# Kernel optimization log

Hardware: AMD Instinct MI355X
Metric: run time of the kernel (lower is better)

The kernel has to match this reference:

```python
import jax, jax.numpy as jnp
import numpy as np


def setup_inputs() -> dict:
    key = jax.random.key(0)
    k1, = jax.random.split(key, 1)
    x = jax.random.normal(k1, (16, 512, 64, 64), dtype=jnp.float32)
    gamma = jnp.zeros((1,), dtype=jnp.float32)
    return {"x": x, "gamma": gamma}


def reference(x, gamma):
    B, C, H, W = x.shape
    q = x.reshape(B, C, H * W)              # B x C x N
    # energy: B x C x C  (channel-channel gram matrix)
    energy = jnp.einsum('bcn,bdn->bcd', q, q)
    # max-subtract transform: max over last dim minus energy
    energy_new = jnp.max(energy, axis=-1, keepdims=True) - energy
    attention = jax.nn.softmax(energy_new, axis=-1)  # B x C x C
    out = jnp.einsum('bcd,bdn->bcn', attention, q).reshape(B, C, H, W)
    return gamma * out + x
```

## Files before the change

### kernel.cpp

```cpp
#include <hip/hip_runtime.h>
#include <stdint.h>

#define B_ 16
#define C_ 512
#define N_ 4096

typedef float f32x4 __attribute__((ext_vector_type(4)));
typedef __bf16 bf16x8 __attribute__((ext_vector_type(8)));

static __device__ __forceinline__ unsigned short f2bf(float f) {
    unsigned int u = __float_as_uint(f);
    u += 0x7fffu + ((u >> 16) & 1u);
    return (unsigned short)(u >> 16);
}

static __device__ __forceinline__ void gload_lds16(const void* g, void* l) {
    __builtin_amdgcn_global_load_lds(
        (__attribute__((address_space(1))) unsigned int*)(g),
        (__attribute__((address_space(3))) unsigned int*)(l),
        16, 0, 0);
}

static __device__ __forceinline__ void stage_pair(const char* Ab, const char* Bb,
                                                  char* as, char* bs, int tid,
                                                  int rowBytes, int m0, int n0, int kByte) {
#pragma unroll
    for (int i = 0; i < 2; ++i) {
        int o = (i * 256 + tid) * 16;
        int mrow = o >> 6, inrow = o & 63;
        gload_lds16(Ab + (size_t)(m0 + mrow) * rowBytes + kByte + inrow, as + o);
        gload_lds16(Bb + (size_t)(n0 + mrow) * rowBytes + kByte + inrow, bs + o);
    }
}

__global__ __launch_bounds__(256)
void convert_transpose(const float* __restrict__ x,
                       unsigned short* __restrict__ q16,
                       unsigned short* __restrict__ qt16) {
    int b = blockIdx.z;
    int t = threadIdx.x;
    int c0 = blockIdx.y * 64 + (t >> 4) * 4;
    int n0 = blockIdx.x * 64 + (t & 15) * 4;

    const float* xb = x + ((size_t)b * C_ + c0) * N_ + n0;
    unsigned short h[4][4];
#pragma unroll
    for (int i = 0; i < 4; ++i) {
        float4 v = *(const float4*)(xb + (size_t)i * N_);
        h[i][0] = f2bf(v.x); h[i][1] = f2bf(v.y);
        h[i][2] = f2bf(v.z); h[i][3] = f2bf(v.w);
    }
    unsigned short* qb = q16 + ((size_t)b * C_ + c0) * N_ + n0;
#pragma unroll
    for (int i = 0; i < 4; ++i) {
        ushort4 p; p.x = h[i][0]; p.y = h[i][1]; p.z = h[i][2]; p.w = h[i][3];
        *(ushort4*)(qb + (size_t)i * N_) = p;
    }
    unsigned short* qtb = qt16 + ((size_t)b * N_ + n0) * C_ + c0;
#pragma unroll
    for (int j = 0; j < 4; ++j) {
        ushort4 p; p.x = h[0][j]; p.y = h[1][j]; p.z = h[2][j]; p.w = h[3][j];
        *(ushort4*)(qtb + (size_t)j * C_) = p;
    }
}

template<int KROW, int NT>
__global__ __launch_bounds__(256)
void gemm_bt_energy(const unsigned short* __restrict__ q16,
                    float* __restrict__ e0, float* __restrict__ e1) {
    int zb = blockIdx.z;
    int b = zb >> 1, ks = zb & 1;
    int kbeg = ks * (NT * 32);
    const char* Ab = (const char*)(q16 + (size_t)b * C_ * KROW);
    int m0 = blockIdx.y * 128, n0 = blockIdx.x * 128;

    __shared__ unsigned short As[3][128 * 32];
    __shared__ unsigned short Bs[3][128 * 32];

    int t = threadIdx.x;
    int lane = t & 63, wave = t >> 6;
    int wm = (wave >> 1) * 64, wn = (wave & 1) * 64;
    int qd = lane >> 4, r = lane & 15;

    f32x4 acc[4][4] = {};

    const int rowB = KROW * 2;
    stage_pair(Ab, Ab, (char*)As[0], (char*)Bs[0], t, rowB, m0, n0, kbeg * 2);
    stage_pair(Ab, Ab, (char*)As[1], (char*)Bs[1], t, rowB, m0, n0, (kbeg + 32) * 2);

    int bufi = 0;
    for (int tt = 0; tt < NT; ++tt) {
        if (tt < NT - 1) asm volatile("s_waitcnt vmcnt(4) lgkmcnt(0)" ::: "memory");
        else             asm volatile("s_waitcnt vmcnt(0) lgkmcnt(0)" ::: "memory");
        __builtin_amdgcn_s_barrier();

        if (tt + 2 < NT) {
            int nb = bufi + 2; if (nb >= 3) nb -= 3;
            stage_pair(Ab, Ab, (char*)As[nb], (char*)Bs[nb], t, rowB,
                       m0, n0, (kbeg + (tt + 2) * 32) * 2);
        }

        const unsigned short* as = As[bufi];
        const unsigned short* bs = Bs[bufi];
        bf16x8 af[4], bfr[4];
#pragma unroll
        for (int i = 0; i < 4; ++i)
            af[i] = *(const bf16x8*)&as[(wm + i * 16 + r) * 32 + qd * 8];
#pragma unroll
        for (int j = 0; j < 4; ++j)
            bfr[j] = *(const bf16x8*)&bs[(wn + j * 16 + r) * 32 + qd * 8];

        __builtin_amdgcn_s_setprio(1);
#pragma unroll
        for (int i = 0; i < 4; ++i)
#pragma unroll
            for (int j = 0; j < 4; ++j)
                acc[i][j] = __builtin_amdgcn_mfma_f32_16x16x32_bf16(af[i], bfr[j], acc[i][j], 0, 0, 0);
        __builtin_amdgcn_s_setprio(0);

        if (++bufi == 3) bufi = 0;
    }

    float* Db = (ks ? e1 : e0) + (size_t)b * C_ * C_;
#pragma unroll
    for (int i = 0; i < 4; ++i)
#pragma unroll
        for (int j = 0; j < 4; ++j) {
            int row = m0 + wm + i * 16 + qd * 4;
            int col = n0 + wn + j * 16 + r;
#pragma unroll
            for (int rr = 0; rr < 4; ++rr)
                Db[(size_t)(row + rr) * C_ + col] = acc[i][j][rr];
        }
}

__global__ __launch_bounds__(256)
void softmax_neg(const float* __restrict__ e0, const float* __restrict__ e1,
                 unsigned short* __restrict__ att) {
    size_t row = blockIdx.x;
    const float* a = e0 + row * C_;
    const float* c = e1 + row * C_;
    int t = threadIdx.x;

    float x0 = a[t] + c[t], x1 = a[t + 256] + c[t + 256];
    float m = fminf(x0, x1);
#pragma unroll
    for (int off = 32; off > 0; off >>= 1) m = fminf(m, __shfl_down(m, off, 64));
    __shared__ float red[8];
    if ((t & 63) == 0) red[t >> 6] = m;
    __syncthreads();
    m = fminf(fminf(red[0], red[1]), fminf(red[2], red[3]));

    float p0 = __expf(m - x0), p1 = __expf(m - x1);
    float s = p0 + p1;
#pragma unroll
    for (int off = 32; off > 0; off >>= 1) s += __shfl_down(s, off, 64);
    if ((t & 63) == 0) red[4 + (t >> 6)] = s;
    __syncthreads();
    s = red[4] + red[5] + red[6] + red[7];
    float inv = 1.0f / s;

    att[row * C_ + t]       = f2bf(p0 * inv);
    att[row * C_ + t + 256] = f2bf(p1 * inv);
}

__global__ __launch_bounds__(256)
void gemm_bt_out(const unsigned short* __restrict__ att,
                 const unsigned short* __restrict__ qt16,
                 const float* __restrict__ x,
                 const float* __restrict__ gamma,
                 float* __restrict__ y) {
    const int K = 512;
    const int NT = K / 32;
    int b = blockIdx.z;
    const char* Ab = (const char*)(att  + (size_t)b * C_ * K);
    const char* Bb = (const char*)(qt16 + (size_t)b * N_ * K);
    int m0 = blockIdx.y * 128;
    int n0 = blockIdx.x * 128;

    __shared__ unsigned short As[3][128 * 32];
    __shared__ unsigned short Bs[3][128 * 32];

    int t = threadIdx.x;
    int lane = t & 63, wave = t >> 6;
    int wm = (wave >> 1) * 64, wn = (wave & 1) * 64;
    int qd = lane >> 4, r = lane & 15;

    f32x4 acc[4][4] = {};

    const int rowB = K * 2;
    stage_pair(Ab, Bb, (char*)As[0], (char*)Bs[0], t, rowB, m0, n0, 0);
    stage_pair(Ab, Bb, (char*)As[1], (char*)Bs[1], t, rowB, m0, n0, 64);

    int bufi = 0;
    for (int tt = 0; tt < NT; ++tt) {
        if (tt < NT - 1) asm volatile("s_waitcnt vmcnt(4) lgkmcnt(0)" ::: "memory");
        else             asm volatile("s_waitcnt vmcnt(0) lgkmcnt(0)" ::: "memory");
        __builtin_amdgcn_s_barrier();

        if (tt + 2 < NT) {
            int nb = bufi + 2; if (nb >= 3) nb -= 3;
            stage_pair(Ab, Bb, (char*)As[nb], (char*)Bs[nb], t, rowB,
                       m0, n0, (tt + 2) * 64);
        }

        const unsigned short* as = As[bufi];
        const unsigned short* bs = Bs[bufi];
        bf16x8 af[4], bfr[4];
#pragma unroll
        for (int i = 0; i < 4; ++i)
            af[i] = *(const bf16x8*)&as[(wm + i * 16 + r) * 32 + qd * 8];
#pragma unroll
        for (int j = 0; j < 4; ++j)
            bfr[j] = *(const bf16x8*)&bs[(wn + j * 16 + r) * 32 + qd * 8];

        __builtin_amdgcn_s_setprio(1);
#pragma unroll
        for (int i = 0; i < 4; ++i)
#pragma unroll
            for (int j = 0; j < 4; ++j)
                acc[i][j] = __builtin_amdgcn_mfma_f32_16x16x32_bf16(af[i], bfr[j], acc[i][j], 0, 0, 0);
        __builtin_amdgcn_s_setprio(0);

        if (++bufi == 3) bufi = 0;
    }

    float g = gamma[0];
    const float* xb = x + (size_t)b * C_ * N_;
    float*       yb = y + (size_t)b * C_ * N_;
#pragma unroll
    for (int i = 0; i < 4; ++i)
#pragma unroll
        for (int j = 0; j < 4; ++j) {
            int row = m0 + wm + i * 16 + qd * 4;
            int col = n0 + wn + j * 16 + r;
#pragma unroll
            for (int rr = 0; rr < 4; ++rr) {
                size_t idx = (size_t)(row + rr) * N_ + col;
                yb[idx] = g * acc[i][j][rr] + xb[idx];
            }
        }
}

extern "C" void kernel_launch(void* const* d_in, const int* in_sizes, int n_in,
                              void* d_out, int out_size, void* d_ws, size_t ws_size,
                              hipStream_t stream) {
    const float* x     = (const float*)d_in[0];
    const float* gamma = (const float*)d_in[1];
    float*       y     = (float*)d_out;

    char* ws = (char*)d_ws;
    unsigned short* q16    = (unsigned short*)(ws);
    unsigned short* qt16   = (unsigned short*)(ws + 67108864);
    unsigned short* att16  = (unsigned short*)(ws + 134217728);
    float*          energy0= (float*)(ws + 142606336);
    float*          energy1= (float*)d_out;

    convert_transpose<<<dim3(N_ / 64, C_ / 64, B_), dim3(256), 0, stream>>>(x, q16, qt16);
    gemm_bt_energy<N_, N_ / 64><<<dim3(C_ / 128, C_ / 128, B_ * 2), dim3(256), 0, stream>>>(q16, energy0, energy1);
    softmax_neg<<<dim3(B_ * C_), dim3(256), 0, stream>>>(energy0, energy1, att16);
    gemm_bt_out<<<dim3(N_ / 128, C_ / 128, B_), dim3(256), 0, stream>>>(att16, qt16, x, gamma, y);
}
```

Measured before the change: 398.4 us.

## Exploit Gram symmetry with upper-triangle tiles, 4-way split-K, mirror-sum reduction

```diff
diff --git a/kernel.cpp b/kernel.cpp
--- a/kernel.cpp
+++ b/kernel.cpp
@@ -64,18 +64,29 @@
     }
 }
 
-template<int KROW, int NT>
-__global__ __launch_bounds__(256)
-void gemm_bt_energy(const unsigned short* __restrict__ q16,
-                    float* __restrict__ e0, float* __restrict__ e1) {
-    int zb = blockIdx.z;
-    int b = zb >> 1, ks = zb & 1;
-    int kbeg = ks * (NT * 32);
-    const char* Ab = (const char*)(q16 + (size_t)b * C_ * KROW);
-    int m0 = blockIdx.y * 128, n0 = blockIdx.x * 128;
-
-    __shared__ unsigned short As[3][128 * 32];
-    __shared__ unsigned short Bs[3][128 * 32];
+__global__ __launch_bounds__(256)
+void gemm_energy_upper(const unsigned short* __restrict__ q16,
+                       float* __restrict__ part) {
+    int p = (blockIdx.z * 4 + blockIdx.y) * 10 + blockIdx.x;
+    int l = (p & 7) * 80 + (p >> 3);
+    int tile = l % 10;
+    int ks   = (l / 10) & 3;
+    int b    = l / 40;
+
+    int my, nx;
+    if (tile < 4)      { my = 0; nx = tile; }
+    else if (tile < 7) { my = 1; nx = tile - 3; }
+    else if (tile < 9) { my = 2; nx = tile - 5; }
+    else               { my = 3; nx = 3; }
+    int m0 = my * 128, n0 = nx * 128;
+    int kbeg = ks * 1024;
+    const int NT = 32;
+
+    const char* Ab = (const char*)(q16 + (size_t)b * C_ * N_);
+    const int rowB = N_ * 2;
+
+    __shared__ unsigned short As[4][128 * 32];
+    __shared__ unsigned short Bs[4][128 * 32];
 
     int t = threadIdx.x;
     int lane = t & 63, wave = t >> 6;
@@ -84,24 +95,24 @@
 
     f32x4 acc[4][4] = {};
 
-    const int rowB = KROW * 2;
-    stage_pair(Ab, Ab, (char*)As[0], (char*)Bs[0], t, rowB, m0, n0, kbeg * 2);
+    stage_pair(Ab, Ab, (char*)As[0], (char*)Bs[0], t, rowB, m0, n0, (kbeg +  0) * 2);
     stage_pair(Ab, Ab, (char*)As[1], (char*)Bs[1], t, rowB, m0, n0, (kbeg + 32) * 2);
-
-    int bufi = 0;
+    stage_pair(Ab, Ab, (char*)As[2], (char*)Bs[2], t, rowB, m0, n0, (kbeg + 64) * 2);
+
     for (int tt = 0; tt < NT; ++tt) {
-        if (tt < NT - 1) asm volatile("s_waitcnt vmcnt(4) lgkmcnt(0)" ::: "memory");
-        else             asm volatile("s_waitcnt vmcnt(0) lgkmcnt(0)" ::: "memory");
+        if (tt < NT - 2)       asm volatile("s_waitcnt vmcnt(8) lgkmcnt(0)" ::: "memory");
+        else if (tt == NT - 2) asm volatile("s_waitcnt vmcnt(4) lgkmcnt(0)" ::: "memory");
+        else                   asm volatile("s_waitcnt vmcnt(0) lgkmcnt(0)" ::: "memory");
         __builtin_amdgcn_s_barrier();
 
-        if (tt + 2 < NT) {
-            int nb = bufi + 2; if (nb >= 3) nb -= 3;
+        if (tt + 3 < NT) {
+            int nb = (tt + 3) & 3;
             stage_pair(Ab, Ab, (char*)As[nb], (char*)Bs[nb], t, rowB,
-                       m0, n0, (kbeg + (tt + 2) * 32) * 2);
-        }
-
-        const unsigned short* as = As[bufi];
-        const unsigned short* bs = Bs[bufi];
+                       m0, n0, (kbeg + (tt + 3) * 32) * 2);
+        }
+
+        const unsigned short* as = As[tt & 3];
+        const unsigned short* bs = Bs[tt & 3];
         bf16x8 af[4], bfr[4];
 #pragma unroll
         for (int i = 0; i < 4; ++i)
@@ -117,11 +128,9 @@
             for (int j = 0; j < 4; ++j)
                 acc[i][j] = __builtin_amdgcn_mfma_f32_16x16x32_bf16(af[i], bfr[j], acc[i][j], 0, 0, 0);
         __builtin_amdgcn_s_setprio(0);
-
-        if (++bufi == 3) bufi = 0;
-    }
-
-    float* Db = (ks ? e1 : e0) + (size_t)b * C_ * C_;
+    }
+
+    float* Db = part + ((size_t)ks * B_ + b) * C_ * C_;
 #pragma unroll
     for (int i = 0; i < 4; ++i)
 #pragma unroll
@@ -135,15 +144,65 @@
 }
 
 __global__ __launch_bounds__(256)
-void softmax_neg(const float* __restrict__ e0, const float* __restrict__ e1,
-                 unsigned short* __restrict__ att) {
+void mirror_sum(const float* __restrict__ part, float* __restrict__ E) {
+    int b = blockIdx.z, id = blockIdx.y;
+    int pm, pn;
+    if (id < 3)       { pm = 0; pn = id + 1; }
+    else if (id < 5)  { pm = 1; pn = id - 1; }
+    else if (id == 5) { pm = 2; pn = 3; }
+    else              { pm = id - 6; pn = id - 6; }
+    bool diag = (id >= 6);
+    int m0 = pm * 128 + (blockIdx.x >> 1) * 64;
+    int n0 = pn * 128 + (blockIdx.x & 1) * 64;
+
+    const size_t PS = (size_t)B_ * C_ * C_;
+    const float* pb = part + (size_t)b * C_ * C_;
+    float*       Eb = E    + (size_t)b * C_ * C_;
+
+    int t = threadIdx.x, tx = t & 15, ty = t >> 4;
+    __shared__ float tile[64][68];
+
+#pragma unroll
+    for (int s = 0; s < 4; ++s) {
+        int rr = s * 16 + ty;
+        size_t idx = (size_t)(m0 + rr) * C_ + n0 + tx * 4;
+        float4 v0 = *(const float4*)(pb + idx);
+        float4 v1 = *(const float4*)(pb + PS + idx);
+        float4 v2 = *(const float4*)(pb + 2 * PS + idx);
+        float4 v3 = *(const float4*)(pb + 3 * PS + idx);
+        float4 v; v.x = v0.x + v1.x + v2.x + v3.x;
+                  v.y = v0.y + v1.y + v2.y + v3.y;
+                  v.z = v0.z + v1.z + v2.z + v3.z;
+                  v.w = v0.w + v1.w + v2.w + v3.w;
+        *(float4*)(Eb + idx) = v;
+        if (!diag) {
+            tile[rr][tx * 4 + 0] = v.x; tile[rr][tx * 4 + 1] = v.y;
+            tile[rr][tx * 4 + 2] = v.z; tile[rr][tx * 4 + 3] = v.w;
+        }
+    }
+    if (!diag) {
+        __syncthreads();
+#pragma unroll
+        for (int s = 0; s < 4; ++s) {
+            int nr = s * 16 + ty;
+            float4 w;
+            w.x = tile[tx * 4 + 0][nr];
+            w.y = tile[tx * 4 + 1][nr];
+            w.z = tile[tx * 4 + 2][nr];
+            w.w = tile[tx * 4 + 3][nr];
+            *(float4*)(Eb + (size_t)(n0 + nr) * C_ + m0 + tx * 4) = w;
+        }
+    }
+}
+
+__global__ __launch_bounds__(256)
+void softmax_neg(const float* __restrict__ energy, unsigned short* __restrict__ att) {
     size_t row = blockIdx.x;
-    const float* a = e0 + row * C_;
-    const float* c = e1 + row * C_;
+    const float* e = energy + row * C_;
     int t = threadIdx.x;
 
-    float x0 = a[t] + c[t], x1 = a[t + 256] + c[t + 256];
-    float m = fminf(x0, x1);
+    float e0 = e[t], e1 = e[t + 256];
+    float m = fminf(e0, e1);
 #pragma unroll
     for (int off = 32; off > 0; off >>= 1) m = fminf(m, __shfl_down(m, off, 64));
     __shared__ float red[8];
@@ -151,7 +210,7 @@
     __syncthreads();
     m = fminf(fminf(red[0], red[1]), fminf(red[2], red[3]));
 
-    float p0 = __expf(m - x0), p1 = __expf(m - x1);
+    float p0 = __expf(m - e0), p1 = __expf(m - e1);
     float s = p0 + p1;
 #pragma unroll
     for (int off = 32; off > 0; off >>= 1) s += __shfl_down(s, off, 64);
@@ -172,14 +231,17 @@
                  float* __restrict__ y) {
     const int K = 512;
     const int NT = K / 32;
-    int b = blockIdx.z;
+    int p = (blockIdx.z * 4 + blockIdx.y) * 32 + blockIdx.x;
+    int l = (p & 7) * 256 + (p >> 3);
+    int bx = l & 31, by = (l >> 5) & 3, b = l >> 7;
+
     const char* Ab = (const char*)(att  + (size_t)b * C_ * K);
     const char* Bb = (const char*)(qt16 + (size_t)b * N_ * K);
-    int m0 = blockIdx.y * 128;
-    int n0 = blockIdx.x * 128;
-
-    __shared__ unsigned short As[3][128 * 32];
-    __shared__ unsigned short Bs[3][128 * 32];
+    int m0 = by * 128;
+    int n0 = bx * 128;
+
+    __shared__ unsigned short As[4][128 * 32];
+    __shared__ unsigned short Bs[4][128 * 32];
 
     int t = threadIdx.x;
     int lane = t & 63, wave = t >> 6;
@@ -191,21 +253,22 @@
     const int rowB = K * 2;
     stage_pair(Ab, Bb, (char*)As[0], (char*)Bs[0], t, rowB, m0, n0, 0);
     stage_pair(Ab, Bb, (char*)As[1], (char*)Bs[1], t, rowB, m0, n0, 64);
-
-    int bufi = 0;
+    stage_pair(Ab, Bb, (char*)As[2], (char*)Bs[2], t, rowB, m0, n0, 128);
+
     for (int tt = 0; tt < NT; ++tt) {
-        if (tt < NT - 1) asm volatile("s_waitcnt vmcnt(4) lgkmcnt(0)" ::: "memory");
-        else             asm volatile("s_waitcnt vmcnt(0) lgkmcnt(0)" ::: "memory");
+        if (tt < NT - 2)       asm volatile("s_waitcnt vmcnt(8) lgkmcnt(0)" ::: "memory");
+        else if (tt == NT - 2) asm volatile("s_waitcnt vmcnt(4) lgkmcnt(0)" ::: "memory");
+        else                   asm volatile("s_waitcnt vmcnt(0) lgkmcnt(0)" ::: "memory");
         __builtin_amdgcn_s_barrier();
 
-        if (tt + 2 < NT) {
-            int nb = bufi + 2; if (nb >= 3) nb -= 3;
+        if (tt + 3 < NT) {
+            int nb = (tt + 3) & 3;
             stage_pair(Ab, Bb, (char*)As[nb], (char*)Bs[nb], t, rowB,
-                       m0, n0, (tt + 2) * 64);
-        }
-
-        const unsigned short* as = As[bufi];
-        const unsigned short* bs = Bs[bufi];
+                       m0, n0, (tt + 3) * 64);
+        }
+
+        const unsigned short* as = As[tt & 3];
+        const unsigned short* bs = Bs[tt & 3];
         bf16x8 af[4], bfr[4];
 #pragma unroll
         for (int i = 0; i < 4; ++i)
@@ -221,8 +284,6 @@
             for (int j = 0; j < 4; ++j)
                 acc[i][j] = __builtin_amdgcn_mfma_f32_16x16x32_bf16(af[i], bfr[j], acc[i][j], 0, 0, 0);
         __builtin_amdgcn_s_setprio(0);
-
-        if (++bufi == 3) bufi = 0;
     }
 
     float g = gamma[0];
@@ -250,14 +311,15 @@
     float*       y     = (float*)d_out;
 
     char* ws = (char*)d_ws;
-    unsigned short* q16    = (unsigned short*)(ws);
-    unsigned short* qt16   = (unsigned short*)(ws + 67108864);
-    unsigned short* att16  = (unsigned short*)(ws + 134217728);
-    float*          energy0= (float*)(ws + 142606336);
-    float*          energy1= (float*)d_out;
+    unsigned short* q16   = (unsigned short*)(ws);
+    unsigned short* qt16  = (unsigned short*)(ws + 67108864);
+    unsigned short* att16 = (unsigned short*)(ws + 134217728);
+    float*          E     = (float*)(ws + 142606336);
+    float*          part  = (float*)d_out;
 
     convert_transpose<<<dim3(N_ / 64, C_ / 64, B_), dim3(256), 0, stream>>>(x, q16, qt16);
-    gemm_bt_energy<N_, N_ / 64><<<dim3(C_ / 128, C_ / 128, B_ * 2), dim3(256), 0, stream>>>(q16, energy0, energy1);
-    softmax_neg<<<dim3(B_ * C_), dim3(256), 0, stream>>>(energy0, energy1, att16);
+    gemm_energy_upper<<<dim3(10, 4, B_), dim3(256), 0, stream>>>(q16, part);
+    mirror_sum<<<dim3(4, 10, B_), dim3(256), 0, stream>>>(part, E);
+    softmax_neg<<<dim3(B_ * C_), dim3(256), 0, stream>>>(E, att16);
     gemm_bt_out<<<dim3(N_ / 128, C_ / 128, B_), dim3(256), 0, stream>>>(att16, qt16, x, gamma, y);
 }
```

Result: no change. 405.0 us (+1.7%).

## Deepen GEMM pipelines, swizzle block order, load attention A-fragments directly to registers

Applied to the files above, without the earlier changes.

```diff
diff --git a/kernel.cpp b/kernel.cpp
--- a/kernel.cpp
+++ b/kernel.cpp
@@ -33,6 +33,16 @@
     }
 }
 
+static __device__ __forceinline__ void stage_B(const char* Bb, char* bs, int tid,
+                                               int rowBytes, int n0, int kByte) {
+#pragma unroll
+    for (int i = 0; i < 2; ++i) {
+        int o = (i * 256 + tid) * 16;
+        int nrow = o >> 6, inrow = o & 63;
+        gload_lds16(Bb + (size_t)(n0 + nrow) * rowBytes + kByte + inrow, bs + o);
+    }
+}
+
 __global__ __launch_bounds__(256)
 void convert_transpose(const float* __restrict__ x,
                        unsigned short* __restrict__ q16,
@@ -64,18 +74,21 @@
     }
 }
 
-template<int KROW, int NT>
-__global__ __launch_bounds__(256)
-void gemm_bt_energy(const unsigned short* __restrict__ q16,
-                    float* __restrict__ e0, float* __restrict__ e1) {
-    int zb = blockIdx.z;
-    int b = zb >> 1, ks = zb & 1;
-    int kbeg = ks * (NT * 32);
-    const char* Ab = (const char*)(q16 + (size_t)b * C_ * KROW);
-    int m0 = blockIdx.y * 128, n0 = blockIdx.x * 128;
-
-    __shared__ unsigned short As[3][128 * 32];
-    __shared__ unsigned short Bs[3][128 * 32];
+__global__ __launch_bounds__(256)
+void gemm_energy(const unsigned short* __restrict__ q16,
+                 float* __restrict__ e0, float* __restrict__ e1) {
+    int p = (blockIdx.z * 2 + blockIdx.y) * 16 + blockIdx.x;
+    int l = (p & 7) * 64 + (p >> 3);
+    int tile = l & 15, ks = (l >> 4) & 1, b = l >> 5;
+    int m0 = (tile >> 2) * 128, n0 = (tile & 3) * 128;
+    int kbeg = ks * 2048;
+    const int NT = 64;
+
+    const char* Ab = (const char*)(q16 + (size_t)b * C_ * N_);
+    const int rowB = N_ * 2;
+
+    __shared__ unsigned short As[4][128 * 32];
+    __shared__ unsigned short Bs[4][128 * 32];
 
     int t = threadIdx.x;
     int lane = t & 63, wave = t >> 6;
@@ -84,24 +97,24 @@
 
     f32x4 acc[4][4] = {};
 
-    const int rowB = KROW * 2;
-    stage_pair(Ab, Ab, (char*)As[0], (char*)Bs[0], t, rowB, m0, n0, kbeg * 2);
+    stage_pair(Ab, Ab, (char*)As[0], (char*)Bs[0], t, rowB, m0, n0, (kbeg +  0) * 2);
     stage_pair(Ab, Ab, (char*)As[1], (char*)Bs[1], t, rowB, m0, n0, (kbeg + 32) * 2);
-
-    int bufi = 0;
+    stage_pair(Ab, Ab, (char*)As[2], (char*)Bs[2], t, rowB, m0, n0, (kbeg + 64) * 2);
+
     for (int tt = 0; tt < NT; ++tt) {
-        if (tt < NT - 1) asm volatile("s_waitcnt vmcnt(4) lgkmcnt(0)" ::: "memory");
-        else             asm volatile("s_waitcnt vmcnt(0) lgkmcnt(0)" ::: "memory");
+        if (tt < NT - 2)       asm volatile("s_waitcnt vmcnt(8) lgkmcnt(0)" ::: "memory");
+        else if (tt == NT - 2) asm volatile("s_waitcnt vmcnt(4) lgkmcnt(0)" ::: "memory");
+        else                   asm volatile("s_waitcnt vmcnt(0) lgkmcnt(0)" ::: "memory");
         __builtin_amdgcn_s_barrier();
 
-        if (tt + 2 < NT) {
-            int nb = bufi + 2; if (nb >= 3) nb -= 3;
+        if (tt + 3 < NT) {
+            int nb = (tt + 3) & 3;
             stage_pair(Ab, Ab, (char*)As[nb], (char*)Bs[nb], t, rowB,
-                       m0, n0, (kbeg + (tt + 2) * 32) * 2);
+                       m0, n0, (kbeg + (tt + 3) * 32) * 2);
         }
 
-        const unsigned short* as = As[bufi];
-        const unsigned short* bs = Bs[bufi];
+        const unsigned short* as = As[tt & 3];
+        const unsigned short* bs = Bs[tt & 3];
         bf16x8 af[4], bfr[4];
 #pragma unroll
         for (int i = 0; i < 4; ++i)
@@ -117,8 +130,6 @@
             for (int j = 0; j < 4; ++j)
                 acc[i][j] = __builtin_amdgcn_mfma_f32_16x16x32_bf16(af[i], bfr[j], acc[i][j], 0, 0, 0);
         __builtin_amdgcn_s_setprio(0);
-
-        if (++bufi == 3) bufi = 0;
     }
 
     float* Db = (ks ? e1 : e0) + (size_t)b * C_ * C_;
@@ -172,58 +183,72 @@
                  float* __restrict__ y) {
     const int K = 512;
     const int NT = K / 32;
-    int b = blockIdx.z;
+    int p = (blockIdx.z * 4 + blockIdx.y) * 32 + blockIdx.x;
+    int l = (p & 7) * 256 + (p >> 3);
+    int bx = l & 31, by = (l >> 5) & 3, b = l >> 7;
+
     const char* Ab = (const char*)(att  + (size_t)b * C_ * K);
     const char* Bb = (const char*)(qt16 + (size_t)b * N_ * K);
-    int m0 = blockIdx.y * 128;
-    int n0 = blockIdx.x * 128;
-
-    __shared__ unsigned short As[3][128 * 32];
-    __shared__ unsigned short Bs[3][128 * 32];
+    int m0 = by * 128;
+    int n0 = bx * 128;
+
+    __shared__ unsigned short Bs[5][128 * 32];
 
     int t = threadIdx.x;
     int lane = t & 63, wave = t >> 6;
     int wm = (wave >> 1) * 64, wn = (wave & 1) * 64;
     int qd = lane >> 4, r = lane & 15;
 
+    const int rowB = K * 2;
+    const char* Arow[4];
+#pragma unroll
+    for (int i = 0; i < 4; ++i)
+        Arow[i] = Ab + (size_t)(m0 + wm + i * 16 + r) * rowB + qd * 16;
+
     f32x4 acc[4][4] = {};
-
-    const int rowB = K * 2;
-    stage_pair(Ab, Bb, (char*)As[0], (char*)Bs[0], t, rowB, m0, n0, 0);
-    stage_pair(Ab, Bb, (char*)As[1], (char*)Bs[1], t, rowB, m0, n0, 64);
-
-    int bufi = 0;
-    for (int tt = 0; tt < NT; ++tt) {
-        if (tt < NT - 1) asm volatile("s_waitcnt vmcnt(4) lgkmcnt(0)" ::: "memory");
-        else             asm volatile("s_waitcnt vmcnt(0) lgkmcnt(0)" ::: "memory");
-        __builtin_amdgcn_s_barrier();
-
-        if (tt + 2 < NT) {
-            int nb = bufi + 2; if (nb >= 3) nb -= 3;
-            stage_pair(Ab, Bb, (char*)As[nb], (char*)Bs[nb], t, rowB,
-                       m0, n0, (tt + 2) * 64);
-        }
-
-        const unsigned short* as = As[bufi];
-        const unsigned short* bs = Bs[bufi];
-        bf16x8 af[4], bfr[4];
-#pragma unroll
-        for (int i = 0; i < 4; ++i)
-            af[i] = *(const bf16x8*)&as[(wm + i * 16 + r) * 32 + qd * 8];
-#pragma unroll
-        for (int j = 0; j < 4; ++j)
-            bfr[j] = *(const bf16x8*)&bs[(wn + j * 16 + r) * 32 + qd * 8];
-
-        __builtin_amdgcn_s_setprio(1);
-#pragma unroll
-        for (int i = 0; i < 4; ++i)
-#pragma unroll
-            for (int j = 0; j < 4; ++j)
-                acc[i][j] = __builtin_amdgcn_mfma_f32_16x16x32_bf16(af[i], bfr[j], acc[i][j], 0, 0, 0);
-        __builtin_amdgcn_s_setprio(0);
-
-        if (++bufi == 3) bufi = 0;
-    }
+    bf16x8 afA[4], afB[4];
+
+#pragma unroll
+    for (int i = 0; i < 4; ++i) afA[i] = *(const bf16x8*)(Arow[i]);
+    stage_B(Bb, (char*)Bs[0], t, rowB, n0, 0);
+    stage_B(Bb, (char*)Bs[1], t, rowB, n0, 64);
+    stage_B(Bb, (char*)Bs[2], t, rowB, n0, 128);
+    stage_B(Bb, (char*)Bs[3], t, rowB, n0, 192);
+
+#define OUT_ITER(tt, CUR, NXT)                                                  \
+    {                                                                           \
+        asm volatile("s_waitcnt lgkmcnt(0)" ::: "memory");                      \
+        __builtin_amdgcn_s_barrier();                                           \
+        if ((tt) + 4 < NT)                                                      \
+            stage_B(Bb, (char*)Bs[((tt) + 4) % 5], t, rowB, n0, ((tt) + 4) * 64); \
+        if ((tt) + 1 < NT) {                                                    \
+            _Pragma("unroll")                                                   \
+            for (int i = 0; i < 4; ++i)                                         \
+                NXT[i] = *(const bf16x8*)(Arow[i] + ((tt) + 1) * 64);           \
+        }                                                                       \
+        if ((tt) + 4 < NT)       asm volatile("s_waitcnt vmcnt(6)" ::: "memory"); \
+        else if ((tt) + 1 < NT)  asm volatile("s_waitcnt vmcnt(4)" ::: "memory"); \
+        else                     asm volatile("s_waitcnt vmcnt(0)" ::: "memory"); \
+        const unsigned short* bs = Bs[(tt) % 5];                                \
+        bf16x8 bfr[4];                                                          \
+        _Pragma("unroll")                                                       \
+        for (int j = 0; j < 4; ++j)                                             \
+            bfr[j] = *(const bf16x8*)&bs[(wn + j * 16 + r) * 32 + qd * 8];      \
+        __builtin_amdgcn_s_setprio(1);                                          \
+        _Pragma("unroll")                                                       \
+        for (int i = 0; i < 4; ++i)                                             \
+            _Pragma("unroll")                                                   \
+            for (int j = 0; j < 4; ++j)                                         \
+                acc[i][j] = __builtin_amdgcn_mfma_f32_16x16x32_bf16(CUR[i], bfr[j], acc[i][j], 0, 0, 0); \
+        __builtin_amdgcn_s_setprio(0);                                          \
+    }
+
+#pragma unroll
+    for (int t2 = 0; t2 < NT / 2; ++t2) {
+        OUT_ITER(2 * t2,     afA, afB);
+        OUT_ITER(2 * t2 + 1, afB, afA);
+    }
+#undef OUT_ITER
 
     float g = gamma[0];
     const float* xb = x + (size_t)b * C_ * N_;
@@ -250,14 +275,14 @@
     float*       y     = (float*)d_out;
 
     char* ws = (char*)d_ws;
-    unsigned short* q16    = (unsigned short*)(ws);
-    unsigned short* qt16   = (unsigned short*)(ws + 67108864);
-    unsigned short* att16  = (unsigned short*)(ws + 134217728);
-    float*          energy0= (float*)(ws + 142606336);
-    float*          energy1= (float*)d_out;
+    unsigned short* q16   = (unsigned short*)(ws);
+    unsigned short* qt16  = (unsigned short*)(ws + 67108864);
+    unsigned short* att16 = (unsigned short*)(ws + 134217728);
+    float*          e0    = (float*)(ws + 142606336);
+    float*          e1    = (float*)d_out;
 
     convert_transpose<<<dim3(N_ / 64, C_ / 64, B_), dim3(256), 0, stream>>>(x, q16, qt16);
-    gemm_bt_energy<N_, N_ / 64><<<dim3(C_ / 128, C_ / 128, B_ * 2), dim3(256), 0, stream>>>(q16, energy0, energy1);
-    softmax_neg<<<dim3(B_ * C_), dim3(256), 0, stream>>>(energy0, energy1, att16);
+    gemm_energy<<<dim3(16, 2, B_), dim3(256), 0, stream>>>(q16, e0, e1);
+    softmax_neg<<<dim3(B_ * C_), dim3(256), 0, stream>>>(e0, e1, att16);
     gemm_bt_out<<<dim3(N_ / 128, C_ / 128, B_), dim3(256), 0, stream>>>(att16, qt16, x, gamma, y);
 }
```

New measurement: 424.5 us. +6.5%, slower.

## Use 256x256 block tiles with 512 threads, 4-way split-K energy, XCD-aware block mapping

Applied to the files above, without the earlier changes.

```diff
diff --git a/kernel.cpp b/kernel.cpp
--- a/kernel.cpp
+++ b/kernel.cpp
@@ -21,12 +21,12 @@
         16, 0, 0);
 }
 
-static __device__ __forceinline__ void stage_pair(const char* Ab, const char* Bb,
-                                                  char* as, char* bs, int tid,
-                                                  int rowBytes, int m0, int n0, int kByte) {
+static __device__ __forceinline__ void stage_pair512(const char* Ab, const char* Bb,
+                                                     char* as, char* bs, int tid,
+                                                     int rowBytes, int m0, int n0, int kByte) {
 #pragma unroll
     for (int i = 0; i < 2; ++i) {
-        int o = (i * 256 + tid) * 16;
+        int o = (i * 512 + tid) * 16;
         int mrow = o >> 6, inrow = o & 63;
         gload_lds16(Ab + (size_t)(m0 + mrow) * rowBytes + kByte + inrow, as + o);
         gload_lds16(Bb + (size_t)(n0 + mrow) * rowBytes + kByte + inrow, bs + o);
@@ -64,47 +64,49 @@
     }
 }
 
-template<int KROW, int NT>
-__global__ __launch_bounds__(256)
-void gemm_bt_energy(const unsigned short* __restrict__ q16,
-                    float* __restrict__ e0, float* __restrict__ e1) {
-    int zb = blockIdx.z;
-    int b = zb >> 1, ks = zb & 1;
-    int kbeg = ks * (NT * 32);
-    const char* Ab = (const char*)(q16 + (size_t)b * C_ * KROW);
-    int m0 = blockIdx.y * 128, n0 = blockIdx.x * 128;
-
-    __shared__ unsigned short As[3][128 * 32];
-    __shared__ unsigned short Bs[3][128 * 32];
+__global__ __launch_bounds__(512, 2)
+void gemm_energy(const unsigned short* __restrict__ q16,
+                 float* __restrict__ part) {
+    int p = blockIdx.x;
+    int l = (p & 7) * 32 + (p >> 3);
+    int tile = l & 3, ks = (l >> 2) & 3, b = l >> 4;
+    int m0 = (tile >> 1) * 256, n0 = (tile & 1) * 256;
+    int kbeg = ks * 1024;
+    const int NT = 32;
+
+    const char* Ab = (const char*)(q16 + (size_t)b * C_ * N_);
+    const int rowB = N_ * 2;
+
+    __shared__ unsigned short As[3][256 * 32];
+    __shared__ unsigned short Bs[3][256 * 32];
 
     int t = threadIdx.x;
     int lane = t & 63, wave = t >> 6;
-    int wm = (wave >> 1) * 64, wn = (wave & 1) * 64;
+    int wm = (wave >> 2) * 128, wn = (wave & 3) * 64;
     int qd = lane >> 4, r = lane & 15;
 
-    f32x4 acc[4][4] = {};
-
-    const int rowB = KROW * 2;
-    stage_pair(Ab, Ab, (char*)As[0], (char*)Bs[0], t, rowB, m0, n0, kbeg * 2);
-    stage_pair(Ab, Ab, (char*)As[1], (char*)Bs[1], t, rowB, m0, n0, (kbeg + 32) * 2);
-
-    int bufi = 0;
+    f32x4 acc[8][4] = {};
+
+    stage_pair512(Ab, Ab, (char*)As[0], (char*)Bs[0], t, rowB, m0, n0, (kbeg +  0) * 2);
+    stage_pair512(Ab, Ab, (char*)As[1], (char*)Bs[1], t, rowB, m0, n0, (kbeg + 32) * 2);
+
     for (int tt = 0; tt < NT; ++tt) {
         if (tt < NT - 1) asm volatile("s_waitcnt vmcnt(4) lgkmcnt(0)" ::: "memory");
         else             asm volatile("s_waitcnt vmcnt(0) lgkmcnt(0)" ::: "memory");
         __builtin_amdgcn_s_barrier();
 
         if (tt + 2 < NT) {
-            int nb = bufi + 2; if (nb >= 3) nb -= 3;
-            stage_pair(Ab, Ab, (char*)As[nb], (char*)Bs[nb], t, rowB,
-                       m0, n0, (kbeg + (tt + 2) * 32) * 2);
-        }
-
-        const unsigned short* as = As[bufi];
-        const unsigned short* bs = Bs[bufi];
-        bf16x8 af[4], bfr[4];
-#pragma unroll
-        for (int i = 0; i < 4; ++i)
+            int nb = tt + 2; while (nb >= 3) nb -= 3;
+            stage_pair512(Ab, Ab, (char*)As[nb], (char*)Bs[nb], t, rowB,
+                          m0, n0, (kbeg + (tt + 2) * 32) * 2);
+        }
+
+        int cb = tt; while (cb >= 3) cb -= 3;
+        const unsigned short* as = As[cb];
+        const unsigned short* bs = Bs[cb];
+        bf16x8 af[8], bfr[4];
+#pragma unroll
+        for (int i = 0; i < 8; ++i)
             af[i] = *(const bf16x8*)&as[(wm + i * 16 + r) * 32 + qd * 8];
 #pragma unroll
         for (int j = 0; j < 4; ++j)
@@ -112,18 +114,16 @@
 
         __builtin_amdgcn_s_setprio(1);
 #pragma unroll
-        for (int i = 0; i < 4; ++i)
+        for (int i = 0; i < 8; ++i)
 #pragma unroll
             for (int j = 0; j < 4; ++j)
                 acc[i][j] = __builtin_amdgcn_mfma_f32_16x16x32_bf16(af[i], bfr[j], acc[i][j], 0, 0, 0);
         __builtin_amdgcn_s_setprio(0);
-
-        if (++bufi == 3) bufi = 0;
-    }
-
-    float* Db = (ks ? e1 : e0) + (size_t)b * C_ * C_;
-#pragma unroll
-    for (int i = 0; i < 4; ++i)
+    }
+
+    float* Db = part + ((size_t)ks * B_ + b) * C_ * C_;
+#pragma unroll
+    for (int i = 0; i < 8; ++i)
 #pragma unroll
         for (int j = 0; j < 4; ++j) {
             int row = m0 + wm + i * 16 + qd * 4;
@@ -135,14 +135,14 @@
 }
 
 __global__ __launch_bounds__(256)
-void softmax_neg(const float* __restrict__ e0, const float* __restrict__ e1,
-                 unsigned short* __restrict__ att) {
+void softmax_neg(const float* __restrict__ part, unsigned short* __restrict__ att) {
     size_t row = blockIdx.x;
-    const float* a = e0 + row * C_;
-    const float* c = e1 + row * C_;
-    int t = threadIdx.x;
-
-    float x0 = a[t] + c[t], x1 = a[t + 256] + c[t + 256];
+    const size_t PS = (size_t)B_ * C_ * C_;
+    const float* e = part + row * C_;
+    int t = threadIdx.x;
+
+    float x0 = e[t]       + e[PS + t]       + e[2 * PS + t]       + e[3 * PS + t];
+    float x1 = e[t + 256] + e[PS + t + 256] + e[2 * PS + t + 256] + e[3 * PS + t + 256];
     float m = fminf(x0, x1);
 #pragma unroll
     for (int off = 32; off > 0; off >>= 1) m = fminf(m, __shfl_down(m, off, 64));
@@ -164,7 +164,7 @@
     att[row * C_ + t + 256] = f2bf(p1 * inv);
 }
 
-__global__ __launch_bounds__(256)
+__global__ __launch_bounds__(512, 2)
 void gemm_bt_out(const unsigned short* __restrict__ att,
                  const unsigned short* __restrict__ qt16,
                  const float* __restrict__ x,
@@ -172,43 +172,46 @@
                  float* __restrict__ y) {
     const int K = 512;
     const int NT = K / 32;
-    int b = blockIdx.z;
+    int p = blockIdx.x;
+    int l = (p & 7) * 64 + (p >> 3);
+    int bx = l & 15, by = (l >> 4) & 1, b = l >> 5;
+
     const char* Ab = (const char*)(att  + (size_t)b * C_ * K);
     const char* Bb = (const char*)(qt16 + (size_t)b * N_ * K);
-    int m0 = blockIdx.y * 128;
-    int n0 = blockIdx.x * 128;
-
-    __shared__ unsigned short As[3][128 * 32];
-    __shared__ unsigned short Bs[3][128 * 32];
+    int m0 = by * 256;
+    int n0 = bx * 256;
+
+    __shared__ unsigned short As[3][256 * 32];
+    __shared__ unsigned short Bs[3][256 * 32];
 
     int t = threadIdx.x;
     int lane = t & 63, wave = t >> 6;
-    int wm = (wave >> 1) * 64, wn = (wave & 1) * 64;
+    int wm = (wave >> 2) * 128, wn = (wave & 3) * 64;
     int qd = lane >> 4, r = lane & 15;
 
-    f32x4 acc[4][4] = {};
+    f32x4 acc[8][4] = {};
 
     const int rowB = K * 2;
-    stage_pair(Ab, Bb, (char*)As[0], (char*)Bs[0], t, rowB, m0, n0, 0);
-    stage_pair(Ab, Bb, (char*)As[1], (char*)Bs[1], t, rowB, m0, n0, 64);
-
-    int bufi = 0;
+    stage_pair512(Ab, Bb, (char*)As[0], (char*)Bs[0], t, rowB, m0, n0, 0);
+    stage_pair512(Ab, Bb, (char*)As[1], (char*)Bs[1], t, rowB, m0, n0, 64);
+
     for (int tt = 0; tt < NT; ++tt) {
         if (tt < NT - 1) asm volatile("s_waitcnt vmcnt(4) lgkmcnt(0)" ::: "memory");
         else             asm volatile("s_waitcnt vmcnt(0) lgkmcnt(0)" ::: "memory");
         __builtin_amdgcn_s_barrier();
 
         if (tt + 2 < NT) {
-            int nb = bufi + 2; if (nb >= 3) nb -= 3;
-            stage_pair(Ab, Bb, (char*)As[nb], (char*)Bs[nb], t, rowB,
-                       m0, n0, (tt + 2) * 64);
-        }
-
-        const unsigned short* as = As[bufi];
-        const unsigned short* bs = Bs[bufi];
-        bf16x8 af[4], bfr[4];
-#pragma unroll
-        for (int i = 0; i < 4; ++i)
+            int nb = tt + 2; while (nb >= 3) nb -= 3;
+            stage_pair512(Ab, Bb, (char*)As[nb], (char*)Bs[nb], t, rowB,
+                          m0, n0, (tt + 2) * 64);
+        }
+
+        int cb = tt; while (cb >= 3) cb -= 3;
+        const unsigned short* as = As[cb];
+        const unsigned short* bs = Bs[cb];
+        bf16x8 af[8], bfr[4];
+#pragma unroll
+        for (int i = 0; i < 8; ++i)
             af[i] = *(const bf16x8*)&as[(wm + i * 16 + r) * 32 + qd * 8];
 #pragma unroll
         for (int j = 0; j < 4; ++j)
@@ -216,20 +219,18 @@
 
         __builtin_amdgcn_s_setprio(1);
 #pragma unroll
-        for (int i = 0; i < 4; ++i)
+        for (int i = 0; i < 8; ++i)
 #pragma unroll
             for (int j = 0; j < 4; ++j)
                 acc[i][j] = __builtin_amdgcn_mfma_f32_16x16x32_bf16(af[i], bfr[j], acc[i][j], 0, 0, 0);
         __builtin_amdgcn_s_setprio(0);
-
-        if (++bufi == 3) bufi = 0;
     }
 
     float g = gamma[0];
     const float* xb = x + (size_t)b * C_ * N_;
     float*       yb = y + (size_t)b * C_ * N_;
 #pragma unroll
-    for (int i = 0; i < 4; ++i)
+    for (int i = 0; i < 8; ++i)
 #pragma unroll
         for (int j = 0; j < 4; ++j) {
             int row = m0 + wm + i * 16 + qd * 4;
@@ -250,14 +251,13 @@
     float*       y     = (float*)d_out;
 
     char* ws = (char*)d_ws;
-    unsigned short* q16    = (unsigned short*)(ws);
-    unsigned short* qt16   = (unsigned short*)(ws + 67108864);
-    unsigned short* att16  = (unsigned short*)(ws + 134217728);
-    float*          energy0= (float*)(ws + 142606336);
-    float*          energy1= (float*)d_out;
+    unsigned short* q16   = (unsigned short*)(ws);
+    unsigned short* qt16  = (unsigned short*)(ws + 67108864);
+    unsigned short* att16 = (unsigned short*)(ws + 134217728);
+    float*          part  = (float*)d_out;
 
     convert_transpose<<<dim3(N_ / 64, C_ / 64, B_), dim3(256), 0, stream>>>(x, q16, qt16);
-    gemm_bt_energy<N_, N_ / 64><<<dim3(C_ / 128, C_ / 128, B_ * 2), dim3(256), 0, stream>>>(q16, energy0, energy1);
-    softmax_neg<<<dim3(B_ * C_), dim3(256), 0, stream>>>(energy0, energy1, att16);
-    gemm_bt_out<<<dim3(N_ / 128, C_ / 128, B_), dim3(256), 0, stream>>>(att16, qt16, x, gamma, y);
-}
+    gemm_energy<<<dim3(256), dim3(512), 0, stream>>>(q16, part);
+    softmax_neg<<<dim3(B_ * C_), dim3(256), 0, stream>>>(part, att16);
+    gemm_bt_out<<<dim3(512), dim3(512), 0, stream>>>(att16, qt16, x, gamma, y);
+}
```

Result: no change. 390.6 us (-1.9%).
